# Performance work log

Hardware: AMD Instinct MI355X
Metric: run time of the kernel (lower is better)

Reference implementation:

```python
import jax, jax.numpy as jnp
import numpy as np

B, S, D_IN, D_INT, D_OUT, E, K_SYN = 2, 2048, 2048, 2048, 2048, 4, 512
GROUPS = D_INT // 8  # Conv1d groups

def setup_inputs() -> dict:
    key = jax.random.key(0)
    ks = jax.random.split(key, 20)
    n = lambda k, sh, std: jax.random.normal(k, sh, dtype=jnp.float32) * std
    d = {}
    d['x'] = jax.random.normal(ks[0], (B, S, D_IN), dtype=jnp.float32)
    d['syntax_ids'] = jax.random.randint(ks[1], (B, S), 0, K_SYN, dtype=jnp.int32)
    d['W_in'] = n(ks[2], (D_IN, D_INT), D_IN ** -0.5)
    d['b_in'] = jnp.zeros((D_INT,), jnp.float32)
    d['W_syn_emb'] = n(ks[3], (K_SYN, D_INT // 4), 0.02)
    d['W_syn'] = n(ks[4], (D_INT + D_INT // 4, D_INT), 0.02)
    d['b_syn'] = jnp.zeros((D_INT,), jnp.float32)
    d['W_gate'] = n(ks[5], (D_INT, 1), 0.02)
    d['b_gate'] = jnp.zeros((1,), jnp.float32)
    d['W_router'] = n(ks[6], (D_INT, E), 0.02)
    d['b_router'] = jnp.zeros((E,), jnp.float32)
    d['W_e1'] = n(ks[7], (E, D_INT, 2 * D_INT), 0.02)
    d['b_e1'] = jnp.zeros((E, 2 * D_INT), jnp.float32)
    d['W_e2'] = n(ks[8], (E, 2 * D_INT, D_INT), 0.02)
    d['b_e2'] = jnp.zeros((E, D_INT), jnp.float32)
    d['W_ctx'] = n(ks[9], (D_INT, D_INT), D_INT ** -0.5)
    d['b_ctx'] = jnp.zeros((D_INT,), jnp.float32)
    fan = 8 * 3 + 8 * 3
    lim = float(np.sqrt(6.0 / fan))
    d['conv_w'] = jax.random.uniform(ks[10], (D_INT, 8, 3), jnp.float32, -lim, lim)
    d['conv_b'] = jnp.zeros((D_INT,), jnp.float32)
    d['W_out'] = n(ks[11], (D_INT, D_OUT), D_INT ** -0.5)
    d['b_out'] = jnp.zeros((D_OUT,), jnp.float32)
    return d

def _forward(x, syntax_ids, W_in, b_in, W_syn_emb, W_syn, b_syn, W_gate, b_gate,
             W_router, b_router, W_e1, b_e1, W_e2, b_e2, W_ctx, b_ctx,
             conv_w, conv_b, W_out, b_out):
    # input projection + SiLU (dropout is identity in eval / p=0)
    h = jax.nn.silu(jnp.einsum('bsi,id->bsd', x, W_in) + b_in)
    # syntax-aware projection
    se = W_syn_emb[syntax_ids]                       # [B,S,D/4] gather
    h = jnp.einsum('bsc,cd->bsd', jnp.concatenate([h, se], axis=-1), W_syn) + b_syn
    # adaptive computation gate
    gate = jax.nn.sigmoid(jnp.einsum('bsd,do->bso', h, W_gate) + b_gate)
    h = h * gate
    # dense mixture-of-experts combine (softmax router weights)
    probs = jax.nn.softmax(jnp.einsum('bsd,de->bse', h, W_router) + b_router, axis=-1)
    eh = jax.nn.silu(jnp.einsum('bsd,edf->bsef', h, W_e1) + b_e1)   # [B,S,E,2D]
    eo = jnp.einsum('bsef,efd->bsed', eh, W_e2) + b_e2              # [B,S,E,D]
    h = h + jnp.einsum('bsed,bse->bsd', eo, probs)
    # code-specific: context linear + grouped Conv1d pattern extractor
    ctx = jnp.einsum('bsd,df->bsf', h, W_ctx) + b_ctx
    hc = jnp.transpose(h, (0, 2, 1))  # [B,D,S]
    pat = jax.lax.conv_general_dilated(
        hc, conv_w, window_strides=(1,), padding=((1, 1),),
        dimension_numbers=('NCH', 'OIH', 'NCH'), feature_group_count=GROUPS)
    pat = jnp.transpose(pat + conv_b[None, :, None], (0, 2, 1))
    h = h + ctx + pat
    out = jnp.einsum('bsd,do->bso', h, W_out) + b_out
    return out + x  # residual (input_dim == output_dim)

def reference(x, syntax_ids, W_in, b_in, W_syn_emb, W_syn, b_syn, W_gate, b_gate,
              W_router, b_router, W_e1, b_e1, W_e2, b_e2, W_ctx, b_ctx,
              conv_w, conv_b, W_out, b_out):
    return _forward(x, syntax_ids, W_in, b_in, W_syn_emb, W_syn, b_syn, W_gate,
                    b_gate, W_router, b_router, W_e1, b_e1, W_e2, b_e2,
                    W_ctx, b_ctx, conv_w, conv_b, W_out, b_out)
```

## Files before the change

kernel.cpp:

```cpp
#include <hip/hip_runtime.h>

typedef __attribute__((ext_vector_type(8))) short short8;
typedef __attribute__((ext_vector_type(4))) float floatx4;

__device__ __forceinline__ float b2f(ushort us) {
    union { unsigned u; float f; } v; v.u = ((unsigned)us) << 16; return v.f;
}
__device__ __forceinline__ ushort f2b(float f) {
    union { float f; unsigned u; } v; v.f = f;
    unsigned r = (v.u + 0x7fffu + ((v.u >> 16) & 1u)) >> 16;
    return (ushort)r;
}
__device__ __forceinline__ float ldany(const void* p, long i, int bf) {
    return bf ? b2f(((const ushort*)p)[i]) : ((const float*)p)[i];
}
__device__ __forceinline__ void async16(const ushort* g, ushort* l) {
    __builtin_amdgcn_global_load_lds((const __attribute__((address_space(1))) void*)g,
                                     (__attribute__((address_space(3))) void*)l,
                                     16, 0, 0);
}

__global__ void detect_dtype(const unsigned* __restrict__ w, int* __restrict__ flag)
{
    if (threadIdx.x == 0 && blockIdx.x == 0) {
        int votes = 0;
        for (int i = 0; i < 256; i++) {
            unsigned e = (w[i] >> 7) & 0xFFu;
            if (e >= 112u && e <= 128u) votes++;
        }
        *flag = (votes >= 128) ? 1 : 0;
    }
}

__global__ __launch_bounds__(256) void transpose_any(
    const void* __restrict__ in, long in_off, ushort* __restrict__ out,
    int R, int C, const int* __restrict__ flag)
{
    __shared__ float tile[64][65];
    const int bf = *flag;
    const int t  = threadIdx.x;
    const long r0 = (long)blockIdx.y * 64;
    const long c0 = (long)blockIdx.x * 64;
    const int rl = t >> 4;
    const int cl = (t & 15) * 4;
    #pragma unroll
    for (int p = 0; p < 4; p++) {
        const int r = rl + p * 16;
        const long base = in_off + (r0 + r) * C + c0 + cl;
        if (bf) {
            ushort4 v = *(const ushort4*)((const ushort*)in + base);
            tile[r][cl + 0] = b2f(v.x); tile[r][cl + 1] = b2f(v.y);
            tile[r][cl + 2] = b2f(v.z); tile[r][cl + 3] = b2f(v.w);
        } else {
            float4 v = *(const float4*)((const float*)in + base);
            tile[r][cl + 0] = v.x; tile[r][cl + 1] = v.y;
            tile[r][cl + 2] = v.z; tile[r][cl + 3] = v.w;
        }
    }
    __syncthreads();
    #pragma unroll
    for (int p = 0; p < 4; p++) {
        const int oc = rl + p * 16;
        ushort4 v;
        v.x = f2b(tile[cl + 0][oc]); v.y = f2b(tile[cl + 1][oc]);
        v.z = f2b(tile[cl + 2][oc]); v.w = f2b(tile[cl + 3][oc]);
        *(ushort4*)(out + (c0 + oc) * R + r0 + cl) = v;
    }
}

__global__ void to_bf16_any(const void* __restrict__ in, ushort* __restrict__ out,
                            long n4, const int* __restrict__ flag)
{
    const long i = (long)blockIdx.x * blockDim.x + threadIdx.x;
    if (i >= n4) return;
    const int bf = *flag;
    ushort4 o;
    if (bf) {
        o = ((const ushort4*)in)[i];
    } else {
        float4 v = ((const float4*)in)[i];
        o.x = f2b(v.x); o.y = f2b(v.y); o.z = f2b(v.z); o.w = f2b(v.w);
    }
    ((ushort4*)out)[i] = o;
}

#define EPI_SILU    0
#define EPI_BIAS    1
#define EPI_EXPERT  2
#define EPI_CTX     3
#define EPI_OUT     4
#define EPI_EXPSNAP 5

#define BAR()        __builtin_amdgcn_s_barrier()
#define WAIT_LGKM0() asm volatile("s_waitcnt lgkmcnt(0)" ::: "memory")
#define WAIT_VM6()   asm volatile("s_waitcnt vmcnt(6)" ::: "memory")
#define WAIT_VM5()   asm volatile("s_waitcnt vmcnt(5)" ::: "memory")
#define WAIT_VM0()   asm volatile("s_waitcnt vmcnt(0)" ::: "memory")

#define STAGE_A(BUF, H, KT) do {                                               \
    const long _k0 = (long)(KT) << 6;                                          \
    _Pragma("unroll")                                                          \
    for (int _i = 0; _i < AINSTR; ++_i) {                                      \
        const int _gi   = w + _i * 8;                                          \
        const int _s    = _gi / AHALF_GRP;                                     \
        const int _wg   = _gi % AHALF_GRP;                                     \
        const int _row0 = _s * (BM / 2) + (H) * (BM / 4) + _wg * 8;            \
        const int _grow = _row0 + (lane >> 3);                                 \
        async16(A + (m0 + _grow) * (long)K + _k0 +                             \
                    (((lane & 7) ^ (_grow & 7)) << 3),                         \
                smem + (BUF) * BUFU + _row0 * 64);                             \
    } } while (0)

#define STAGE_B(BUF, H, KT) do {                                               \
    const long _k0 = (long)(KT) << 6;                                          \
    _Pragma("unroll")                                                          \
    for (int _i = 0; _i < 2; ++_i) {                                           \
        const int _gi   = w * 2 + _i;                                          \
        const int _row0 = (_gi >> 2) * 64 + (H) * 32 + (_gi & 3) * 8;          \
        const int _grow = _row0 + (lane >> 3);                                 \
        async16(Bt + (n0 + _grow) * (long)K + _k0 +                            \
                     (((lane & 7) ^ (_grow & 7)) << 3),                        \
                smem + (BUF) * BUFU + BM * 64 + _row0 * 64);                   \
    } } while (0)

#define LOAD_A(BUF, MH) do {                                                   \
    _Pragma("unroll")                                                          \
    for (int _m = 0; _m < MF / 2; ++_m) {                                      \
        const int _row = wm * (BM / 2) + ((MH) * (MF / 2) + _m) * 16 + fr;     \
        _Pragma("unroll")                                                      \
        for (int _ks = 0; _ks < 2; ++_ks)                                      \
            a[_m][_ks] = *(const short8*)(smem + (BUF) * BUFU + _row * 64 +    \
                                          (((_ks * 4 + q) ^ (_row & 7)) << 3));\
    } } while (0)

#define LOAD_B(BUF, NH, BREG) do {                                             \
    _Pragma("unroll")                                                          \
    for (int _n = 0; _n < 2; ++_n) {                                           \
        const int _row = wn * 64 + ((NH) * 2 + _n) * 16 + fr;                  \
        _Pragma("unroll")                                                      \
        for (int _ks = 0; _ks < 2; ++_ks)                                      \
            BREG[_n][_ks] = *(const short8*)(smem + (BUF) * BUFU + BM * 64 +   \
                                             _row * 64 +                       \
                                          (((_ks * 4 + q) ^ (_row & 7)) << 3));\
    } } while (0)

#define MMA(MH, NH, BREG) do {                                                 \
    _Pragma("unroll")                                                          \
    for (int _m = 0; _m < MF / 2; ++_m)                                        \
    _Pragma("unroll")                                                          \
    for (int _n = 0; _n < 2; ++_n)                                             \
    _Pragma("unroll")                                                          \
    for (int _ks = 0; _ks < 2; ++_ks)                                          \
        acc[(MH) * (MF / 2) + _m][(NH) * 2 + _n] =                             \
            __builtin_amdgcn_mfma_f32_16x16x32_bf16(                           \
                a[_m][_ks], BREG[_n][_ks],                                     \
                acc[(MH) * (MF / 2) + _m][(NH) * 2 + _n], 0, 0, 0);            \
    } while (0)

template<int EPI, int MF>
__global__ __launch_bounds__(512, 2) void gemm8(
    const ushort* __restrict__ A, const ushort* __restrict__ Bt,
    int M, int N, int K,
    const void* __restrict__ bias, long bias_off,
    void* __restrict__ out, long ldo,
    float* __restrict__ hacc,
    const float* __restrict__ rowscale,
    const ushort* __restrict__ resid,
    const int* __restrict__ flag)
{
    constexpr int BM        = MF * 32;
    constexpr int AHALF_GRP = BM / 32;
    constexpr int AINSTR    = BM / 128;
    constexpr int BUFU      = (BM + 256) * 64;
    extern __shared__ ushort smem[];

    const int tid  = threadIdx.x;
    const int lane = tid & 63;
    const int w    = tid >> 6;
    const int wm   = w >> 2;
    const int wn   = w & 3;
    const int fr   = lane & 15;
    const int q    = lane >> 4;
    const long m0  = (long)blockIdx.y * BM;
    const long n0  = (long)blockIdx.x * 256;
    const int NT   = K >> 6;

    floatx4 acc[MF][4] = {};
    short8 a[MF / 2][2];
    short8 b0[2][2], b1[2][2];

    STAGE_A(0, 0, 0); STAGE_A(0, 1, 0); STAGE_B(0, 0, 0); STAGE_B(0, 1, 0);
    STAGE_A(1, 0, 1); STAGE_B(1, 0, 1); STAGE_B(1, 1, 1);
    if constexpr (MF == 8) WAIT_VM6(); else WAIT_VM5();
    BAR();

    for (int t = 0; t < NT; ++t) {
        const int cur = t & 1, nxt = cur ^ 1;
        LOAD_A(cur, 0);
        LOAD_B(cur, 0, b0);
        if (t + 1 < NT) STAGE_A(nxt, 1, t + 1);
        BAR(); WAIT_LGKM0();
        __builtin_amdgcn_s_setprio(1); MMA(0, 0, b0); __builtin_amdgcn_s_setprio(0);
        BAR();
        LOAD_B(cur, 1, b1);
        if (t + 2 < NT) STAGE_A(cur, 0, t + 2);
        BAR(); WAIT_LGKM0();
        __builtin_amdgcn_s_setprio(1); MMA(0, 1, b1); __builtin_amdgcn_s_setprio(0);
        BAR();
        LOAD_A(cur, 1);
        if (t + 2 < NT) STAGE_B(cur, 0, t + 2);
        BAR(); WAIT_LGKM0();
        __builtin_amdgcn_s_setprio(1); MMA(1, 1, b1); __builtin_amdgcn_s_setprio(0);
        BAR();
        if (t + 2 < NT) {
            STAGE_B(cur, 1, t + 2);
            if constexpr (MF == 8) WAIT_VM6(); else WAIT_VM5();
        } else {
            WAIT_VM0();
        }
        BAR();
        __builtin_amdgcn_s_setprio(1); MMA(1, 0, b0); __builtin_amdgcn_s_setprio(0);
        BAR();
    }

    const int bf = *flag;
    #pragma unroll
    for (int i = 0; i < MF; ++i) {
        #pragma unroll
        for (int r = 0; r < 4; ++r) {
            const long m = m0 + wm * (BM / 2) + i * 16 + q * 4 + r;
            #pragma unroll
            for (int j = 0; j < 4; ++j) {
                const long n = n0 + wn * 64 + j * 16 + fr;
                float v = acc[i][j][r] + ldany(bias, bias_off + n, bf);
                if (EPI == EPI_SILU) {
                    v = v / (1.f + __expf(-v));
                    ((ushort*)out)[m * ldo + n] = f2b(v);
                } else if (EPI == EPI_BIAS) {
                    ((ushort*)out)[m * ldo + n] = f2b(v);
                } else if (EPI == EPI_EXPERT) {
                    hacc[m * (long)N + n] += rowscale[m * 4] * v;
                } else if (EPI == EPI_EXPSNAP) {
                    const long idx = m * (long)N + n;
                    const float nv = hacc[idx] + rowscale[m * 4] * v;
                    hacc[idx] = nv;
                    ((ushort*)out)[m * ldo + n] = f2b(nv);
                } else if (EPI == EPI_CTX) {
                    hacc[m * (long)N + n] += v;
                } else {
                    v += b2f(resid[m * (long)N + n]);
                    if (bf) ((ushort*)out)[m * ldo + n] = f2b(v);
                    else    ((float*)out)[m * ldo + n]  = v;
                }
            }
        }
    }
}

__global__ void gather_syn(const int* __restrict__ ids, const void* __restrict__ emb,
                           ushort* __restrict__ hA, const int* __restrict__ flag)
{
    const int bf = *flag;
    const long m = blockIdx.x;
    const int id = ids[m];
    const int j = threadIdx.x * 2;
    float a, b;
    if (bf) {
        ushort2 v = *(const ushort2*)((const ushort*)emb + (long)id * 512 + j);
        a = b2f(v.x); b = b2f(v.y);
    } else {
        float2 v = *(const float2*)((const float*)emb + (long)id * 512 + j);
        a = v.x; b = v.y;
    }
    ushort2 o; o.x = f2b(a); o.y = f2b(b);
    *(ushort2*)(hA + m * 2560 + 2048 + j) = o;
}

__global__ __launch_bounds__(256) void gate_router(
    ushort* __restrict__ h2, float* __restrict__ hacc, float* __restrict__ probs,
    const void* __restrict__ Wg, const void* __restrict__ bg,
    const void* __restrict__ Wr, const void* __restrict__ br,
    const int* __restrict__ flag)
{
    const int bf = *flag;
    const long m = blockIdx.x;
    const int t = threadIdx.x;
    const int lane = t & 63;
    const int wv = t >> 6;
    ushort* row = h2 + m * 2048;

    float sg = 0.f, s0 = 0.f, s1 = 0.f, s2 = 0.f, s3 = 0.f;
    for (int k = t; k < 2048; k += 256) {
        const float h = b2f(row[k]);
        sg += h * ldany(Wg, k, bf);
        float r0v, r1v, r2v, r3v;
        if (bf) {
            ushort4 v = *(const ushort4*)((const ushort*)Wr + (long)k * 4);
            r0v = b2f(v.x); r1v = b2f(v.y); r2v = b2f(v.z); r3v = b2f(v.w);
        } else {
            float4 v = *(const float4*)((const float*)Wr + (long)k * 4);
            r0v = v.x; r1v = v.y; r2v = v.z; r3v = v.w;
        }
        s0 += h * r0v; s1 += h * r1v; s2 += h * r2v; s3 += h * r3v;
    }
    #pragma unroll
    for (int off = 32; off > 0; off >>= 1) {
        sg += __shfl_down(sg, off);
        s0 += __shfl_down(s0, off);
        s1 += __shfl_down(s1, off);
        s2 += __shfl_down(s2, off);
        s3 += __shfl_down(s3, off);
    }
    __shared__ float red[4][5];
    __shared__ float gate_bc;
    if (lane == 0) {
        red[wv][0] = sg; red[wv][1] = s0; red[wv][2] = s1;
        red[wv][3] = s2; red[wv][4] = s3;
    }
    __syncthreads();
    if (t == 0) {
        float G = red[0][0] + red[1][0] + red[2][0] + red[3][0];
        float R[4];
        #pragma unroll
        for (int e = 0; e < 4; e++)
            R[e] = red[0][1 + e] + red[1][1 + e] + red[2][1 + e] + red[3][1 + e];
        const float gate = 1.f / (1.f + __expf(-(G + ldany(bg, 0, bf))));
        float lg[4], mx = -1e30f;
        #pragma unroll
        for (int e = 0; e < 4; e++) {
            lg[e] = gate * R[e] + ldany(br, e, bf);
            mx = fmaxf(mx, lg[e]);
        }
        float p[4], s = 0.f;
        #pragma unroll
        for (int e = 0; e < 4; e++) { p[e] = __expf(lg[e] - mx); s += p[e]; }
        #pragma unroll
        for (int e = 0; e < 4; e++) probs[m * 4 + e] = p[e] / s;
        gate_bc = gate;
    }
    __syncthreads();
    const float gate = gate_bc;
    for (int k = t; k < 2048; k += 256) {
        const float v = b2f(row[k]) * gate;
        row[k] = f2b(v);
        hacc[m * 2048 + k] = v;
    }
}

__global__ __launch_bounds__(256) void conv_combine(
    const ushort* __restrict__ h4, const float* __restrict__ hacc,
    const void* __restrict__ cw, const void* __restrict__ cb,
    ushort* __restrict__ h5, const int* __restrict__ flag)
{
    const int S = 2048, D = 2048;
    const int SC = 32;
    const int bf = *flag;
    const int b  = blockIdx.z;
    const int c0 = blockIdx.y * 512;
    const int s0 = blockIdx.x * SC;
    const int t  = threadIdx.x;

    __shared__ ushort tile[(SC + 2) * 512];

    const int cp = 2 * t;
    const int c  = c0 + cp;
    float w0[3][8], w1[3][8];
    #pragma unroll
    for (int kk = 0; kk < 3; kk++)
        #pragma unroll
        for (int ii = 0; ii < 8; ii++) {
            w0[kk][ii] = ldany(cw, (long)c * 24 + ii * 3 + kk, bf);
            w1[kk][ii] = ldany(cw, (long)(c + 1) * 24 + ii * 3 + kk, bf);
        }
    const float bc0 = ldany(cb, c, bf);
    const float bc1 = ldany(cb, c + 1, bf);

    for (int idx = t; idx < (SC + 2) * 64; idx += 256) {
        const int r  = idx >> 6;
        const int ch = (idx & 63) * 8;
        const int s  = s0 - 1 + r;
        short8 v = {};
        if (s >= 0 && s < S)
            v = *(const short8*)(h4 + ((long)b * S + s) * D + c0 + ch);
        *(short8*)(tile + r * 512 + ch) = v;
    }
    __syncthreads();

    const int gc8 = (cp >> 3) * 8;
    for (int sl = 0; sl < SC; ++sl) {
        float p0 = 0.f, p1 = 0.f;
        #pragma unroll
        for (int kk = 0; kk < 3; kk++) {
            short8 v = *(const short8*)(tile + (sl + kk) * 512 + gc8);
            #pragma unroll
            for (int ii = 0; ii < 8; ii++) {
                const float x = b2f((ushort)v[ii]);
                p0 += x * w0[kk][ii];
                p1 += x * w1[kk][ii];
            }
        }
        const long m = (long)b * S + s0 + sl;
        const float2 ha = *(const float2*)(hacc + m * D + c);
        ushort2 o; o.x = f2b(ha.x + bc0 + p0); o.y = f2b(ha.y + bc1 + p1);
        *(ushort2*)(h5 + m * D + c) = o;
    }
}

extern "C" void kernel_launch(void* const* d_in, const int* in_sizes, int n_in,
                              void* d_out, int out_size, void* d_ws, size_t ws_size,
                              hipStream_t stream)
{
    (void)in_sizes; (void)n_in; (void)out_size; (void)ws_size;
    const void* x        = d_in[0];
    const int*  syn      = (const int*)d_in[1];
    const void* W_in     = d_in[2];
    const void* b_in     = d_in[3];
    const void* W_synemb = d_in[4];
    const void* W_syn    = d_in[5];
    const void* b_syn    = d_in[6];
    const void* W_gate   = d_in[7];
    const void* b_gate   = d_in[8];
    const void* W_router = d_in[9];
    const void* b_router = d_in[10];
    const void* W_e1     = d_in[11];
    const void* b_e1     = d_in[12];
    const void* W_e2     = d_in[13];
    const void* b_e2     = d_in[14];
    const void* W_ctx    = d_in[15];
    const void* b_ctx    = d_in[16];
    const void* conv_w   = d_in[17];
    const void* conv_b   = d_in[18];
    const void* W_out    = d_in[19];
    const void* b_out    = d_in[20];

    char* ws = (char*)d_ws;
    int*    flag  = (int*)ws;
    ushort* WT    = (ushort*)(ws + 256);
    ushort* xb    = (ushort*)(ws + 16777472);
    ushort* hA    = (ushort*)(ws + 33554688);
    ushort* eh    = (ushort*)(ws + 16777472);
    ushort* h23   = (ushort*)(ws + 54526208);
    float*  probs = (float*)(ws + 71303424);
    float*  hacc  = (float*)(ws + 71368960);
    const int M = 4096;
    dim3 blk(256);
    const int LDS4 = 98304;
    const int LDS8 = 131072;

    static bool attr_set = false;
    if (!attr_set) {
        (void)hipFuncSetAttribute(reinterpret_cast<const void*>(&gemm8<EPI_SILU,    4>),
                                  hipFuncAttributeMaxDynamicSharedMemorySize, LDS4);
        (void)hipFuncSetAttribute(reinterpret_cast<const void*>(&gemm8<EPI_BIAS,    4>),
                                  hipFuncAttributeMaxDynamicSharedMemorySize, LDS4);
        (void)hipFuncSetAttribute(reinterpret_cast<const void*>(&gemm8<EPI_EXPERT,  4>),
                                  hipFuncAttributeMaxDynamicSharedMemorySize, LDS4);
        (void)hipFuncSetAttribute(reinterpret_cast<const void*>(&gemm8<EPI_EXPSNAP, 4>),
                                  hipFuncAttributeMaxDynamicSharedMemorySize, LDS4);
        (void)hipFuncSetAttribute(reinterpret_cast<const void*>(&gemm8<EPI_CTX,     4>),
                                  hipFuncAttributeMaxDynamicSharedMemorySize, LDS4);
        (void)hipFuncSetAttribute(reinterpret_cast<const void*>(&gemm8<EPI_OUT,     4>),
                                  hipFuncAttributeMaxDynamicSharedMemorySize, LDS4);
        (void)hipFuncSetAttribute(reinterpret_cast<const void*>(&gemm8<EPI_SILU,    8>),
                                  hipFuncAttributeMaxDynamicSharedMemorySize, LDS8);
        attr_set = true;
    }

    detect_dtype<<<dim3(1), dim3(64), 0, stream>>>((const unsigned*)W_in, flag);
    to_bf16_any<<<dim3(8192), blk, 0, stream>>>(x, xb, 2097152L, flag);

    transpose_any<<<dim3(32, 32), blk, 0, stream>>>(W_in, 0, WT, 2048, 2048, flag);
    gemm8<EPI_SILU, 4><<<dim3(8, 32), dim3(512), LDS4, stream>>>(
        xb, WT, M, 2048, 2048, b_in, 0, hA, 2560, nullptr, nullptr, nullptr, flag);
    gather_syn<<<dim3(4096), blk, 0, stream>>>(syn, W_synemb, hA, flag);
    transpose_any<<<dim3(32, 40), blk, 0, stream>>>(W_syn, 0, WT, 2560, 2048, flag);
    gemm8<EPI_BIAS, 4><<<dim3(8, 32), dim3(512), LDS4, stream>>>(
        hA, WT, M, 2048, 2560, b_syn, 0, h23, 2048, nullptr, nullptr, nullptr, flag);
    gate_router<<<dim3(4096), blk, 0, stream>>>(
        h23, hacc, probs, W_gate, b_gate, W_router, b_router, flag);
    for (int e = 0; e < 4; e++) {
        transpose_any<<<dim3(64, 32), blk, 0, stream>>>(
            W_e1, (long)e * 8388608, WT, 2048, 4096, flag);
        gemm8<EPI_SILU, 8><<<dim3(16, 16), dim3(512), LDS8, stream>>>(
            h23, WT, M, 4096, 2048, b_e1, (long)e * 4096, eh, 4096,
            nullptr, nullptr, nullptr, flag);
        transpose_any<<<dim3(32, 64), blk, 0, stream>>>(
            W_e2, (long)e * 8388608, WT, 4096, 2048, flag);
        if (e < 3)
            gemm8<EPI_EXPERT, 4><<<dim3(8, 32), dim3(512), LDS4, stream>>>(
                eh, WT, M, 2048, 4096, b_e2, (long)e * 2048, nullptr, 0,
                hacc, probs + e, nullptr, flag);
        else
            gemm8<EPI_EXPSNAP, 4><<<dim3(8, 32), dim3(512), LDS4, stream>>>(
                eh, WT, M, 2048, 4096, b_e2, (long)e * 2048, h23, 2048,
                hacc, probs + e, nullptr, flag);
    }
    to_bf16_any<<<dim3(8192), blk, 0, stream>>>(x, xb, 2097152L, flag);
    transpose_any<<<dim3(32, 32), blk, 0, stream>>>(W_ctx, 0, WT, 2048, 2048, flag);
    gemm8<EPI_CTX, 4><<<dim3(8, 32), dim3(512), LDS4, stream>>>(
        h23, WT, M, 2048, 2048, b_ctx, 0, nullptr, 0, hacc, nullptr, nullptr, flag);
    conv_combine<<<dim3(64, 4, 2), blk, 0, stream>>>(
        h23, hacc, conv_w, conv_b, hA, flag);
    transpose_any<<<dim3(32, 32), blk, 0, stream>>>(W_out, 0, WT, 2048, 2048, flag);
    gemm8<EPI_OUT, 4><<<dim3(8, 32), dim3(512), LDS4, stream>>>(
        hA, WT, M, 2048, 2048, b_out, 0, d_out, 2048, nullptr, nullptr, xb, flag);
}
```

Baseline: 1.395 ms.

## Split-K expert-down and ctx GEMMs with atomic accumulation into fp32 buffer

The expert second GEMM and the context GEMM now use a 256x256 tile (MF=8) with a 2-way split-K over blockIdx.z, accumulating into the fp32 hidden accumulator with atomicAdd. Only the first K slice adds the bias. The old snapshot epilogue that wrote the bf16 copy of h is replaced by a separate fp32-to-bf16 conversion kernel. The aim is larger tiles with better operand reuse while keeping the grid at 256 blocks. The cost is fp32 atomic traffic, nondeterministic summation order, and an extra elementwise pass.

Result: slower. 1.607 ms (+15.2%).

```diff
diff --git a/kernel.cpp b/kernel.cpp
--- a/kernel.cpp
+++ b/kernel.cpp
@@ -84,12 +84,19 @@
     ((ushort4*)out)[i] = o;
 }
 
+__global__ void f32_to_bf16_4(const float* __restrict__ in, ushort* __restrict__ out, long n4)
+{
+    const long i = (long)blockIdx.x * blockDim.x + threadIdx.x;
+    if (i >= n4) return;
+    float4 v = ((const float4*)in)[i];
+    ushort4 o; o.x = f2b(v.x); o.y = f2b(v.y); o.z = f2b(v.z); o.w = f2b(v.w);
+    ((ushort4*)out)[i] = o;
+}
+
 #define EPI_SILU    0
 #define EPI_BIAS    1
-#define EPI_EXPERT  2
-#define EPI_CTX     3
-#define EPI_OUT     4
-#define EPI_EXPSNAP 5
+#define EPI_OUT     2
+#define EPI_ATOM    3
 
 #define BAR()        __builtin_amdgcn_s_barrier()
 #define WAIT_LGKM0() asm volatile("s_waitcnt lgkmcnt(0)" ::: "memory")
@@ -98,7 +105,7 @@
 #define WAIT_VM0()   asm volatile("s_waitcnt vmcnt(0)" ::: "memory")
 
 #define STAGE_A(BUF, H, KT) do {                                               \
-    const long _k0 = (long)(KT) << 6;                                          \
+    const long _k0 = zoff + ((long)(KT) << 6);                                 \
     _Pragma("unroll")                                                          \
     for (int _i = 0; _i < AINSTR; ++_i) {                                      \
         const int _gi   = w + _i * 8;                                          \
@@ -106,19 +113,19 @@
         const int _wg   = _gi % AHALF_GRP;                                     \
         const int _row0 = _s * (BM / 2) + (H) * (BM / 4) + _wg * 8;            \
         const int _grow = _row0 + (lane >> 3);                                 \
-        async16(A + (m0 + _grow) * (long)K + _k0 +                             \
+        async16(A + (m0 + _grow) * (long)lda + _k0 +                           \
                     (((lane & 7) ^ (_grow & 7)) << 3),                         \
                 smem + (BUF) * BUFU + _row0 * 64);                             \
     } } while (0)
 
 #define STAGE_B(BUF, H, KT) do {                                               \
-    const long _k0 = (long)(KT) << 6;                                          \
+    const long _k0 = zoff + ((long)(KT) << 6);                                 \
     _Pragma("unroll")                                                          \
     for (int _i = 0; _i < 2; ++_i) {                                           \
         const int _gi   = w * 2 + _i;                                          \
         const int _row0 = (_gi >> 2) * 64 + (H) * 32 + (_gi & 3) * 8;          \
         const int _grow = _row0 + (lane >> 3);                                 \
-        async16(Bt + (n0 + _grow) * (long)K + _k0 +                            \
+        async16(Bt + (n0 + _grow) * (long)lda + _k0 +                          \
                      (((lane & 7) ^ (_grow & 7)) << 3),                        \
                 smem + (BUF) * BUFU + BM * 64 + _row0 * 64);                   \
     } } while (0)
@@ -160,7 +167,7 @@
 template<int EPI, int MF>
 __global__ __launch_bounds__(512, 2) void gemm8(
     const ushort* __restrict__ A, const ushort* __restrict__ Bt,
-    int M, int N, int K,
+    int M, int N, int lda, int kslice,
     const void* __restrict__ bias, long bias_off,
     void* __restrict__ out, long ldo,
     float* __restrict__ hacc,
@@ -183,7 +190,8 @@
     const int q    = lane >> 4;
     const long m0  = (long)blockIdx.y * BM;
     const long n0  = (long)blockIdx.x * 256;
-    const int NT   = K >> 6;
+    const long zoff = (long)blockIdx.z * kslice;
+    const int NT   = kslice >> 6;
 
     floatx4 acc[MF][4] = {};
     short8 a[MF / 2][2];
@@ -224,6 +232,7 @@
     }
 
     const int bf = *flag;
+    const bool addb = (EPI != EPI_ATOM) || (blockIdx.z == 0);
     #pragma unroll
     for (int i = 0; i < MF; ++i) {
         #pragma unroll
@@ -232,21 +241,15 @@
             #pragma unroll
             for (int j = 0; j < 4; ++j) {
                 const long n = n0 + wn * 64 + j * 16 + fr;
-                float v = acc[i][j][r] + ldany(bias, bias_off + n, bf);
+                float v = acc[i][j][r] + (addb ? ldany(bias, bias_off + n, bf) : 0.f);
                 if (EPI == EPI_SILU) {
                     v = v / (1.f + __expf(-v));
                     ((ushort*)out)[m * ldo + n] = f2b(v);
                 } else if (EPI == EPI_BIAS) {
                     ((ushort*)out)[m * ldo + n] = f2b(v);
-                } else if (EPI == EPI_EXPERT) {
-                    hacc[m * (long)N + n] += rowscale[m * 4] * v;
-                } else if (EPI == EPI_EXPSNAP) {
-                    const long idx = m * (long)N + n;
-                    const float nv = hacc[idx] + rowscale[m * 4] * v;
-                    hacc[idx] = nv;
-                    ((ushort*)out)[m * ldo + n] = f2b(nv);
-                } else if (EPI == EPI_CTX) {
-                    hacc[m * (long)N + n] += v;
+                } else if (EPI == EPI_ATOM) {
+                    atomicAdd(&hacc[m * (long)N + n],
+                              rowscale ? rowscale[m * 4] * v : v);
                 } else {
                     v += b2f(resid[m * (long)N + n]);
                     if (bf) ((ushort*)out)[m * ldo + n] = f2b(v);
@@ -449,19 +452,15 @@
 
     static bool attr_set = false;
     if (!attr_set) {
-        (void)hipFuncSetAttribute(reinterpret_cast<const void*>(&gemm8<EPI_SILU,    4>),
+        (void)hipFuncSetAttribute(reinterpret_cast<const void*>(&gemm8<EPI_SILU, 4>),
                                   hipFuncAttributeMaxDynamicSharedMemorySize, LDS4);
-        (void)hipFuncSetAttribute(reinterpret_cast<const void*>(&gemm8<EPI_BIAS,    4>),
+        (void)hipFuncSetAttribute(reinterpret_cast<const void*>(&gemm8<EPI_BIAS, 4>),
                                   hipFuncAttributeMaxDynamicSharedMemorySize, LDS4);
-        (void)hipFuncSetAttribute(reinterpret_cast<const void*>(&gemm8<EPI_EXPERT,  4>),
+        (void)hipFuncSetAttribute(reinterpret_cast<const void*>(&gemm8<EPI_OUT,  4>),
                                   hipFuncAttributeMaxDynamicSharedMemorySize, LDS4);
-        (void)hipFuncSetAttribute(reinterpret_cast<const void*>(&gemm8<EPI_EXPSNAP, 4>),
-                                  hipFuncAttributeMaxDynamicSharedMemorySize, LDS4);
-        (void)hipFuncSetAttribute(reinterpret_cast<const void*>(&gemm8<EPI_CTX,     4>),
-                                  hipFuncAttributeMaxDynamicSharedMemorySize, LDS4);
-        (void)hipFuncSetAttribute(reinterpret_cast<const void*>(&gemm8<EPI_OUT,     4>),
-                                  hipFuncAttributeMaxDynamicSharedMemorySize, LDS4);
-        (void)hipFuncSetAttribute(reinterpret_cast<const void*>(&gemm8<EPI_SILU,    8>),
+        (void)hipFuncSetAttribute(reinterpret_cast<const void*>(&gemm8<EPI_SILU, 8>),
+                                  hipFuncAttributeMaxDynamicSharedMemorySize, LDS8);
+        (void)hipFuncSetAttribute(reinterpret_cast<const void*>(&gemm8<EPI_ATOM, 8>),
                                   hipFuncAttributeMaxDynamicSharedMemorySize, LDS8);
         attr_set = true;
     }
@@ -471,37 +470,34 @@
 
     transpose_any<<<dim3(32, 32), blk, 0, stream>>>(W_in, 0, WT, 2048, 2048, flag);
     gemm8<EPI_SILU, 4><<<dim3(8, 32), dim3(512), LDS4, stream>>>(
-        xb, WT, M, 2048, 2048, b_in, 0, hA, 2560, nullptr, nullptr, nullptr, flag);
+        xb, WT, M, 2048, 2048, 2048, b_in, 0, hA, 2560, nullptr, nullptr, nullptr, flag);
     gather_syn<<<dim3(4096), blk, 0, stream>>>(syn, W_synemb, hA, flag);
     transpose_any<<<dim3(32, 40), blk, 0, stream>>>(W_syn, 0, WT, 2560, 2048, flag);
     gemm8<EPI_BIAS, 4><<<dim3(8, 32), dim3(512), LDS4, stream>>>(
-        hA, WT, M, 2048, 2560, b_syn, 0, h23, 2048, nullptr, nullptr, nullptr, flag);
+        hA, WT, M, 2048, 2560, 2560, b_syn, 0, h23, 2048, nullptr, nullptr, nullptr, flag);
     gate_router<<<dim3(4096), blk, 0, stream>>>(
         h23, hacc, probs, W_gate, b_gate, W_router, b_router, flag);
     for (int e = 0; e < 4; e++) {
         transpose_any<<<dim3(64, 32), blk, 0, stream>>>(
             W_e1, (long)e * 8388608, WT, 2048, 4096, flag);
         gemm8<EPI_SILU, 8><<<dim3(16, 16), dim3(512), LDS8, stream>>>(
-            h23, WT, M, 4096, 2048, b_e1, (long)e * 4096, eh, 4096,
+            h23, WT, M, 4096, 2048, 2048, b_e1, (long)e * 4096, eh, 4096,
             nullptr, nullptr, nullptr, flag);
         transpose_any<<<dim3(32, 64), blk, 0, stream>>>(
             W_e2, (long)e * 8388608, WT, 4096, 2048, flag);
-        if (e < 3)
-            gemm8<EPI_EXPERT, 4><<<dim3(8, 32), dim3(512), LDS4, stream>>>(
-                eh, WT, M, 2048, 4096, b_e2, (long)e * 2048, nullptr, 0,
-                hacc, probs + e, nullptr, flag);
-        else
-            gemm8<EPI_EXPSNAP, 4><<<dim3(8, 32), dim3(512), LDS4, stream>>>(
-                eh, WT, M, 2048, 4096, b_e2, (long)e * 2048, h23, 2048,
-                hacc, probs + e, nullptr, flag);
+        gemm8<EPI_ATOM, 8><<<dim3(8, 16, 2), dim3(512), LDS8, stream>>>(
+            eh, WT, M, 2048, 4096, 2048, b_e2, (long)e * 2048, nullptr, 0,
+            hacc, probs + e, nullptr, flag);
     }
     to_bf16_any<<<dim3(8192), blk, 0, stream>>>(x, xb, 2097152L, flag);
+    f32_to_bf16_4<<<dim3(8192), blk, 0, stream>>>(hacc, h23, 2097152L);
     transpose_any<<<dim3(32, 32), blk, 0, stream>>>(W_ctx, 0, WT, 2048, 2048, flag);
-    gemm8<EPI_CTX, 4><<<dim3(8, 32), dim3(512), LDS4, stream>>>(
-        h23, WT, M, 2048, 2048, b_ctx, 0, nullptr, 0, hacc, nullptr, nullptr, flag);
+    gemm8<EPI_ATOM, 8><<<dim3(8, 16, 2), dim3(512), LDS8, stream>>>(
+        h23, WT, M, 2048, 2048, 1024, b_ctx, 0, nullptr, 0,
+        hacc, nullptr, nullptr, flag);
     conv_combine<<<dim3(64, 4, 2), blk, 0, stream>>>(
         h23, hacc, conv_w, conv_b, hA, flag);
     transpose_any<<<dim3(32, 32), blk, 0, stream>>>(W_out, 0, WT, 2048, 2048, flag);
     gemm8<EPI_OUT, 4><<<dim3(8, 32), dim3(512), LDS4, stream>>>(
-        hA, WT, M, 2048, 2048, b_out, 0, d_out, 2048, nullptr, nullptr, xb, flag);
-}
+        hA, WT, M, 2048, 2048, 2048, b_out, 0, d_out, 2048, nullptr, nullptr, xb, flag);
+}
```
